# Kernel tuning notes

Hardware: AMD Instinct MI355X
Metric: run time of the kernel (lower is better)

Reference implementation:

```python
import jax, jax.numpy as jnp
import numpy as np

NA = 3            # anchors per scale
NC = 80           # num classes
THRESH = 0.6      # wh-IoU anchor-match threshold
EPS = 1e-7

ANCHORS_PX = np.array([[12,16],[19,36],[40,28],[36,75],[76,55],[72,146],
                       [142,110],[192,243],[459,401]], dtype=np.float32).reshape(3, 3, 2)


def setup_inputs() -> dict:
    key = jax.random.key(0)
    k1, k2, k3, k4, k5, k6 = jax.random.split(key, 6)
    B, M = 16, 32
    p0 = jax.random.normal(k1, (B, NA * (5 + NC), 80, 80), jnp.float32)
    p1 = jax.random.normal(k2, (B, NA * (5 + NC), 40, 40), jnp.float32)
    p2 = jax.random.normal(k3, (B, NA * (5 + NC), 20, 20), jnp.float32)
    # targets: [B, M, 6] = (img_idx, class in [1,NC], cx, cy, w, h) normalized to [0,1]
    bidx = jnp.broadcast_to(jnp.arange(B, dtype=jnp.float32)[:, None], (B, M))
    cls = jax.random.randint(k4, (B, M), 1, NC + 1).astype(jnp.float32)
    xy = jax.random.uniform(k5, (B, M, 2), minval=0.05, maxval=0.95)
    ka, kj = jax.random.split(k6)
    aidx = jax.random.randint(ka, (B, M), 0, 9)
    base_wh = jnp.asarray(ANCHORS_PX.reshape(9, 2))[aidx] / 640.0
    jitter = jnp.exp(jax.random.uniform(kj, (B, M, 2), minval=-0.15, maxval=0.15))
    wh = base_wh * jitter
    targets = jnp.concatenate([bidx[..., None], cls[..., None], xy, wh], axis=-1)
    return {"p0": p0, "p1": p1, "p2": p2,
            "targets": targets,
            "anchors": jnp.asarray(ANCHORS_PX),
            "image_size": jnp.array([640.0, 640.0], jnp.float32)}


def _bce_logits(x, t):
    # BCEWithLogits, pos_weight=1, elementwise
    return jnp.maximum(x, 0.0) - x * t + jnp.log1p(jnp.exp(-jnp.abs(x)))


def _giou(pbox, tbox):
    # boxes [N,4] in cxcywh
    px1 = pbox[:, 0] - pbox[:, 2] * 0.5
    py1 = pbox[:, 1] - pbox[:, 3] * 0.5
    px2 = pbox[:, 0] + pbox[:, 2] * 0.5
    py2 = pbox[:, 1] + pbox[:, 3] * 0.5
    tx1 = tbox[:, 0] - tbox[:, 2] * 0.5
    ty1 = tbox[:, 1] - tbox[:, 3] * 0.5
    tx2 = tbox[:, 0] + tbox[:, 2] * 0.5
    ty2 = tbox[:, 1] + tbox[:, 3] * 0.5
    iw = jnp.clip(jnp.minimum(px2, tx2) - jnp.maximum(px1, tx1), 0.0)
    ih = jnp.clip(jnp.minimum(py2, ty2) - jnp.maximum(py1, ty1), 0.0)
    inter = iw * ih
    union = pbox[:, 2] * pbox[:, 3] + tbox[:, 2] * tbox[:, 3] - inter + EPS
    iou = inter / union
    cw = jnp.maximum(px2, tx2) - jnp.minimum(px1, tx1)
    ch = jnp.maximum(py2, ty2) - jnp.minimum(py1, ty1)
    c_area = cw * ch + EPS
    return iou - (c_area - union) / c_area


def _scale_losses(pi, tflat, anchors_i, image_size):
    # pi: [B, NA*(5+NC), H, W]; tflat: [N,6]; anchors_i: [NA,2] in pixels
    B = pi.shape[0]
    H, W = pi.shape[-2:]
    stride = image_size / jnp.array([H, W], jnp.float32)          # (sH, sW)
    anchor = anchors_i / stride[::-1][None, :]                    # anchors in grid units (w,h)
    gain = jnp.concatenate([jnp.ones((2,), jnp.float32),
                            (1.0 / stride)[jnp.array([1, 0, 1, 0])]])
    t = tflat * gain                                              # [N,6]
    gwh = t[:, 4:6]
    # wh-IoU matrix [NA, N] -> best anchor per target
    inter = (jnp.minimum(anchor[:, None, 0], gwh[None, :, 0])
             * jnp.minimum(anchor[:, None, 1], gwh[None, :, 1]))
    union = anchor[:, None, 0] * anchor[:, None, 1] + gwh[None, :, 0] * gwh[None, :, 1] - inter
    iou = inter / union
    best = iou.max(0)
    a = iou.argmax(0)
    mask = best > THRESH                                          # fixed-shape mask replaces torch boolean compaction
    maskf = mask.astype(jnp.float32)

    b = jnp.where(mask, t[:, 0].astype(jnp.int32), 0)
    c = t[:, 1].astype(jnp.int32)
    gxy = t[:, 2:4]
    gi = jnp.where(mask, gxy[:, 0].astype(jnp.int32), 0)
    gj = jnp.where(mask, gxy[:, 1].astype(jnp.int32), 0)
    a_s = jnp.where(mask, a, 0)

    pir = pi.reshape(B, NA, 5 + NC, H, W).transpose(0, 1, 3, 4, 2)  # [B,NA,H,W,5+NC]
    ps = pir[b, a_s, gj, gi]                                        # [N,5+NC]
    tobj = jnp.zeros((B, NA, H, W), jnp.float32)
    tobj = tobj.at[b, a_s, gj, gi].max(jax.lax.stop_gradient(maskf))

    pxy = jax.nn.sigmoid(ps[:, 0:2])
    pwh = jnp.minimum(jnp.exp(ps[:, 2:4]), 1000.0) * anchor[a_s]
    pbox = jnp.concatenate([pxy, pwh], 1)
    tbox = jnp.concatenate([gxy % 1.0, t[:, 4:6]], 1)
    giou = _giou(pbox, tbox)
    nb = jnp.maximum(maskf.sum(), 1.0)
    lbox = (maskf * (1.0 - giou)).sum() / nb
    tcls = jax.nn.one_hot(c - 1, NC, dtype=jnp.float32)             # cp=1, cn=0 (eps=0)
    lcls = (maskf[:, None] * _bce_logits(ps[:, 5:], tcls)).sum() / (nb * NC)
    lobj = _bce_logits(pir[..., 4], tobj).mean()
    return lbox, lobj, lcls


def _total_loss(p0, p1, p2, targets, anchors, image_size):
    tflat = targets.reshape(-1, 6)
    lbox = lobj = lcls = jnp.float32(0.0)
    for i, pi in enumerate([p0, p1, p2]):
        lb, lo, lc = _scale_losses(pi, tflat, anchors[i], image_size)
        lbox = lbox + lb
        lobj = lobj + lo
        lcls = lcls + lc
    lbox = lbox * 3.54
    lobj = lobj * 64.3
    lcls = lcls * 37.4
    return lbox + lobj + lcls, lbox, lobj, lcls


def reference(p0, p1, p2, targets, anchors, image_size):
    return _total_loss(p0, p1, p2, targets, anchors, image_size)
```

## Files before the change

kernel.cpp:

```cpp
#include <hip/hip_runtime.h>
#include <math.h>

#define NAANCH 3
#define NCLS 80
#define BATCH 16
#define NTGT 512
#define CH 85

#define V4_S0 76800
#define V4_S1 19200
#define V4_S2 4800
#define V4_TOT (V4_S0 + V4_S1 + V4_S2)
#define OBJ_BLOCKS 197
#define GRID_BLOCKS (3 + OBJ_BLOCKS)

#define WBOX 3.54f
#define WOBJ 64.3f
#define WCLS 37.4f

__device__ __forceinline__ float bce0(float x) {
    return fmaxf(x, 0.0f) + log1pf(expf(-fabsf(x)));
}

__device__ __forceinline__ float wave_sum(float v) {
    for (int off = 32; off > 0; off >>= 1) v += __shfl_down(v, off, 64);
    return v;
}

__global__ void yolo_loss_kernel(const float* __restrict__ p0,
                                 const float* __restrict__ p1,
                                 const float* __restrict__ p2,
                                 const float* __restrict__ targets,
                                 const float* __restrict__ anchors,
                                 const float* __restrict__ image_size,
                                 float* __restrict__ out) {
    const int tid  = threadIdx.x;
    const int lane = tid & 63;
    const int wid  = tid >> 6;

    __shared__ int   sh_key[NTGT];
    __shared__ int   sh_off[NTGT];
    __shared__ int   sh_ci[NTGT];
    __shared__ unsigned char sh_mk[NTGT];
    __shared__ float red[4][8];

    if (blockIdx.x < 3) {
        const int s = blockIdx.x;
        const int j = tid;
        const int H = (s == 0) ? 80 : ((s == 1) ? 40 : 20);
        const int W = H;
        const int HW = H * W;
        const float* pi = (s == 0) ? p0 : ((s == 1) ? p1 : p2);

        const float stride0 = image_size[0] / (float)H;
        const float stride1 = image_size[1] / (float)W;
        const float gx = 1.0f / stride1;
        const float gy = 1.0f / stride0;

        const float t0 = targets[j * 6 + 0];
        const float t1 = targets[j * 6 + 1];
        const float tx = targets[j * 6 + 2] * gx;
        const float ty = targets[j * 6 + 3] * gy;
        const float gw = targets[j * 6 + 4] * gx;
        const float gh = targets[j * 6 + 5] * gy;

        float best = -1.0f; int abest = 0;
        for (int k = 0; k < NAANCH; ++k) {
            float aw = anchors[(s * NAANCH + k) * 2 + 0] / stride1;
            float ah = anchors[(s * NAANCH + k) * 2 + 1] / stride0;
            float inter = fminf(aw, gw) * fminf(ah, gh);
            float uni = aw * ah + gw * gh - inter;
            float iou = inter / uni;
            if (iou > best) { best = iou; abest = k; }
        }
        const bool  mask  = best > 0.6f;
        const float maskf = mask ? 1.0f : 0.0f;

        int b  = mask ? (int)t0 : 0;
        const int c = (int)t1;
        int gi = mask ? (int)tx : 0;
        int gj = mask ? (int)ty : 0;
        const int a_s = mask ? abest : 0;
        gi = min(max(gi, 0), W - 1);
        gj = min(max(gj, 0), H - 1);
        b  = min(max(b, 0), BATCH - 1);

        const int key = ((b * NAANCH + a_s) * H + gj) * W + gi;
        const int off = (b * (NAANCH * CH) + a_s * CH) * HW + gj * W + gi;

        float lbox_t = 0.0f, ps4 = 0.0f;
        if (mask) {
            const float ps0 = pi[off + 0 * HW];
            const float ps1 = pi[off + 1 * HW];
            const float ps2 = pi[off + 2 * HW];
            const float ps3 = pi[off + 3 * HW];
            ps4 = pi[off + 4 * HW];

            const float aw = anchors[(s * NAANCH + a_s) * 2 + 0] / stride1;
            const float ah = anchors[(s * NAANCH + a_s) * 2 + 1] / stride0;

            const float pxc = 1.0f / (1.0f + expf(-ps0));
            const float pyc = 1.0f / (1.0f + expf(-ps1));
            const float pw  = fminf(expf(ps2), 1000.0f) * aw;
            const float ph  = fminf(expf(ps3), 1000.0f) * ah;
            const float txc = tx - floorf(tx);
            const float tyc = ty - floorf(ty);

            const float px1 = pxc - pw * 0.5f, py1 = pyc - ph * 0.5f;
            const float px2 = pxc + pw * 0.5f, py2 = pyc + ph * 0.5f;
            const float qx1 = txc - gw * 0.5f, qy1 = tyc - gh * 0.5f;
            const float qx2 = txc + gw * 0.5f, qy2 = tyc + gh * 0.5f;
            const float iw = fmaxf(fminf(px2, qx2) - fmaxf(px1, qx1), 0.0f);
            const float ih = fmaxf(fminf(py2, qy2) - fmaxf(py1, qy1), 0.0f);
            const float inter = iw * ih;
            const float uni = pw * ph + gw * gh - inter + 1e-7f;
            const float iou = inter / uni;
            const float cw  = fmaxf(px2, qx2) - fminf(px1, qx1);
            const float chh = fmaxf(py2, qy2) - fminf(py1, qy1);
            const float carea = cw * chh + 1e-7f;
            lbox_t = 1.0f - (iou - (carea - uni) / carea);
        }

        sh_key[j] = key;
        sh_off[j] = off;
        sh_ci[j]  = c - 1;
        sh_mk[j]  = mask ? 1 : 0;
        __syncthreads();

        float corr = 0.0f;
        if (mask) {
            bool dup = false;
            for (int j2 = 0; j2 < j; ++j2)
                if (sh_mk[j2] && sh_key[j2] == key) { dup = true; break; }
            if (!dup) corr = -ps4;
        }

        float v0 = wave_sum(lbox_t);
        float v1 = wave_sum(maskf);
        float v2 = wave_sum(corr);
        if (lane == 0) { red[0][wid] = v0; red[1][wid] = v1; red[2][wid] = v2; }
        __syncthreads();

        float lcls_w = 0.0f;
        for (int j2 = wid; j2 < NTGT; j2 += 8) {
            if (!sh_mk[j2]) continue;
            const int toff = sh_off[j2];
            const int ci   = sh_ci[j2];
            const int k1 = lane;
            float x1 = pi[toff + (5 + k1) * HW];
            float c1 = bce0(x1) - ((k1 == ci) ? x1 : 0.0f);
            float c2 = 0.0f;
            if (lane < NCLS - 64) {
                const int k2 = 64 + lane;
                float x2 = pi[toff + (5 + k2) * HW];
                c2 = bce0(x2) - ((k2 == ci) ? x2 : 0.0f);
            }
            float tsum = wave_sum(c1 + c2);
            if (lane == 0) lcls_w += tsum;
        }
        if (lane == 0) red[3][wid] = lcls_w;
        __syncthreads();

        if (tid == 0) {
            float acc[4] = {0.f, 0.f, 0.f, 0.f};
            for (int w = 0; w < 8; ++w) {
                acc[0] += red[0][w]; acc[1] += red[1][w];
                acc[2] += red[2][w]; acc[3] += red[3][w];
            }
            const float Ns = (s == 0) ? 307200.0f : ((s == 1) ? 76800.0f : 19200.0f);
            const float nb = fmaxf(acc[1], 1.0f);
            const float lbox_c = WBOX * (acc[0] / nb);
            const float lobj_c = WOBJ * (acc[2] / Ns);
            const float lcls_c = WCLS * (acc[3] / (nb * (float)NCLS));
            atomicAdd(&out[1], lbox_c);
            atomicAdd(&out[2], lobj_c);
            atomicAdd(&out[3], lcls_c);
            atomicAdd(&out[0], lbox_c + lobj_c + lcls_c);
        }
    } else {
        const int vb = (blockIdx.x - 3) * 512 + tid;
        float a0 = 0.f, a1 = 0.f, a2 = 0.f;
        if (vb < V4_TOT) {
            const float4* addr; int hw4; int sflag;
            if (vb < V4_S0) {
                const int u = vb;
                const int ba = u / 1600;  hw4 = u - ba * 1600;
                const int b = ba / 3, a = ba - 3 * b;
                addr = (const float4*)(p0 + (size_t)((b * NAANCH + a) * CH + 4) * 6400);
                sflag = 0;
            } else if (vb < V4_S0 + V4_S1) {
                const int u = vb - V4_S0;
                const int ba = u / 400;   hw4 = u - ba * 400;
                const int b = ba / 3, a = ba - 3 * b;
                addr = (const float4*)(p1 + (size_t)((b * NAANCH + a) * CH + 4) * 1600);
                sflag = 1;
            } else {
                const int u = vb - V4_S0 - V4_S1;
                const int ba = u / 100;   hw4 = u - ba * 100;
                const int b = ba / 3, a = ba - 3 * b;
                addr = (const float4*)(p2 + (size_t)((b * NAANCH + a) * CH + 4) * 400);
                sflag = 2;
            }
            float4 x = addr[hw4];
            float v = bce0(x.x) + bce0(x.y) + bce0(x.z) + bce0(x.w);
            if (sflag == 0) a0 = v; else if (sflag == 1) a1 = v; else a2 = v;
        }
        a0 = wave_sum(a0); a1 = wave_sum(a1); a2 = wave_sum(a2);
        if (lane == 0) { red[0][wid] = a0; red[1][wid] = a1; red[2][wid] = a2; }
        __syncthreads();
        if (tid == 0) {
            float s0 = 0.f, s1 = 0.f, s2 = 0.f;
            for (int w = 0; w < 8; ++w) { s0 += red[0][w]; s1 += red[1][w]; s2 += red[2][w]; }
            const float lobj_c = WOBJ * (s0 / 307200.0f + s1 / 76800.0f + s2 / 19200.0f);
            atomicAdd(&out[2], lobj_c);
            atomicAdd(&out[0], lobj_c);
        }
    }
}

extern "C" void kernel_launch(void* const* d_in, const int* in_sizes, int n_in,
                              void* d_out, int out_size, void* d_ws, size_t ws_size,
                              hipStream_t stream) {
    const float* p0       = (const float*)d_in[0];
    const float* p1       = (const float*)d_in[1];
    const float* p2       = (const float*)d_in[2];
    const float* targets  = (const float*)d_in[3];
    const float* anchors  = (const float*)d_in[4];
    const float* img_size = (const float*)d_in[5];
    float* out = (float*)d_out;

    yolo_loss_kernel<<<GRID_BLOCKS, 512, 0, stream>>>(p0, p1, p2, targets, anchors, img_size, out);
}
```

Measured before the change: 153.4 us.

## Split class-loss gathers across 96 blocks and double objectness work per thread

Moves the per-target class BCE loss out of the three per-scale blocks into 96 dedicated blocks (32 per scale). Each block recomputes the anchor assignment and handles 16 targets with two independent gathers per wave, so the long serial gather loop no longer sits on the critical path. The objectness blocks now process two float4 vectors per thread, halving their count. Assignment math is recomputed redundantly in every class block, and there are more atomics on the output.

```diff
diff --git a/kernel.cpp b/kernel.cpp
--- a/kernel.cpp
+++ b/kernel.cpp
@@ -11,8 +11,12 @@
 #define V4_S1 19200
 #define V4_S2 4800
 #define V4_TOT (V4_S0 + V4_S1 + V4_S2)
-#define OBJ_BLOCKS 197
-#define GRID_BLOCKS (3 + OBJ_BLOCKS)
+
+#define NCB 32
+#define CLS_BASE 3
+#define OBJ_BASE (CLS_BASE + 3 * NCB)
+#define OBJ_BLOCKS 99
+#define GRID_BLOCKS (OBJ_BASE + OBJ_BLOCKS)
 
 #define WBOX 3.54f
 #define WOBJ 64.3f
@@ -27,13 +31,51 @@
     return v;
 }
 
-__global__ void yolo_loss_kernel(const float* __restrict__ p0,
-                                 const float* __restrict__ p1,
-                                 const float* __restrict__ p2,
-                                 const float* __restrict__ targets,
-                                 const float* __restrict__ anchors,
-                                 const float* __restrict__ image_size,
-                                 float* __restrict__ out) {
+__device__ __forceinline__ void compute_assign(
+    const int s, const int j,
+    const float* __restrict__ targets, const float* __restrict__ anchors,
+    const float inv_sx, const float inv_sy,
+    const int H, const int W, const int HW,
+    bool& mask, int& key, int& off, int& ci, int& a_s,
+    float& tx, float& ty, float& gw, float& gh)
+{
+    const float t0 = targets[j * 6 + 0];
+    const float t1 = targets[j * 6 + 1];
+    tx = targets[j * 6 + 2] * inv_sx;
+    ty = targets[j * 6 + 3] * inv_sy;
+    gw = targets[j * 6 + 4] * inv_sx;
+    gh = targets[j * 6 + 5] * inv_sy;
+
+    float best = -1.0f; int abest = 0;
+    for (int k = 0; k < NAANCH; ++k) {
+        const float aw = anchors[(s * NAANCH + k) * 2 + 0] * inv_sx;
+        const float ah = anchors[(s * NAANCH + k) * 2 + 1] * inv_sy;
+        const float inter = fminf(aw, gw) * fminf(ah, gh);
+        const float uni = aw * ah + gw * gh - inter;
+        const float iou = inter / uni;
+        if (iou > best) { best = iou; abest = k; }
+    }
+    mask = best > 0.6f;
+    int b  = mask ? (int)t0 : 0;
+    ci = (int)t1 - 1;
+    int gi = mask ? (int)tx : 0;
+    int gj = mask ? (int)ty : 0;
+    a_s = mask ? abest : 0;
+    gi = min(max(gi, 0), W - 1);
+    gj = min(max(gj, 0), H - 1);
+    b  = min(max(b, 0), BATCH - 1);
+    key = ((b * NAANCH + a_s) * H + gj) * W + gi;
+    off = (b * (NAANCH * CH) + a_s * CH) * HW + gj * W + gi;
+}
+
+__global__ __launch_bounds__(512)
+void yolo_loss_kernel(const float* __restrict__ p0,
+                      const float* __restrict__ p1,
+                      const float* __restrict__ p2,
+                      const float* __restrict__ targets,
+                      const float* __restrict__ anchors,
+                      const float* __restrict__ image_size,
+                      float* __restrict__ out) {
     const int tid  = threadIdx.x;
     const int lane = tid & 63;
     const int wid  = tid >> 6;
@@ -44,49 +86,20 @@
     __shared__ unsigned char sh_mk[NTGT];
     __shared__ float red[4][8];
 
-    if (blockIdx.x < 3) {
+    if (blockIdx.x < CLS_BASE) {
         const int s = blockIdx.x;
         const int j = tid;
         const int H = (s == 0) ? 80 : ((s == 1) ? 40 : 20);
         const int W = H;
         const int HW = H * W;
         const float* pi = (s == 0) ? p0 : ((s == 1) ? p1 : p2);
-
-        const float stride0 = image_size[0] / (float)H;
-        const float stride1 = image_size[1] / (float)W;
-        const float gx = 1.0f / stride1;
-        const float gy = 1.0f / stride0;
-
-        const float t0 = targets[j * 6 + 0];
-        const float t1 = targets[j * 6 + 1];
-        const float tx = targets[j * 6 + 2] * gx;
-        const float ty = targets[j * 6 + 3] * gy;
-        const float gw = targets[j * 6 + 4] * gx;
-        const float gh = targets[j * 6 + 5] * gy;
-
-        float best = -1.0f; int abest = 0;
-        for (int k = 0; k < NAANCH; ++k) {
-            float aw = anchors[(s * NAANCH + k) * 2 + 0] / stride1;
-            float ah = anchors[(s * NAANCH + k) * 2 + 1] / stride0;
-            float inter = fminf(aw, gw) * fminf(ah, gh);
-            float uni = aw * ah + gw * gh - inter;
-            float iou = inter / uni;
-            if (iou > best) { best = iou; abest = k; }
-        }
-        const bool  mask  = best > 0.6f;
+        const float inv_sx = (float)W / image_size[1];
+        const float inv_sy = (float)H / image_size[0];
+
+        bool mask; int key, off, ci, a_s; float tx, ty, gw, gh;
+        compute_assign(s, j, targets, anchors, inv_sx, inv_sy, H, W, HW,
+                       mask, key, off, ci, a_s, tx, ty, gw, gh);
         const float maskf = mask ? 1.0f : 0.0f;
-
-        int b  = mask ? (int)t0 : 0;
-        const int c = (int)t1;
-        int gi = mask ? (int)tx : 0;
-        int gj = mask ? (int)ty : 0;
-        const int a_s = mask ? abest : 0;
-        gi = min(max(gi, 0), W - 1);
-        gj = min(max(gj, 0), H - 1);
-        b  = min(max(b, 0), BATCH - 1);
-
-        const int key = ((b * NAANCH + a_s) * H + gj) * W + gi;
-        const int off = (b * (NAANCH * CH) + a_s * CH) * HW + gj * W + gi;
 
         float lbox_t = 0.0f, ps4 = 0.0f;
         if (mask) {
@@ -96,8 +109,8 @@
             const float ps3 = pi[off + 3 * HW];
             ps4 = pi[off + 4 * HW];
 
-            const float aw = anchors[(s * NAANCH + a_s) * 2 + 0] / stride1;
-            const float ah = anchors[(s * NAANCH + a_s) * 2 + 1] / stride0;
+            const float aw = anchors[(s * NAANCH + a_s) * 2 + 0] * inv_sx;
+            const float ah = anchors[(s * NAANCH + a_s) * 2 + 1] * inv_sy;
 
             const float pxc = 1.0f / (1.0f + expf(-ps0));
             const float pyc = 1.0f / (1.0f + expf(-ps1));
@@ -122,8 +135,6 @@
         }
 
         sh_key[j] = key;
-        sh_off[j] = off;
-        sh_ci[j]  = c - 1;
         sh_mk[j]  = mask ? 1 : 0;
         __syncthreads();
 
@@ -141,69 +152,110 @@
         if (lane == 0) { red[0][wid] = v0; red[1][wid] = v1; red[2][wid] = v2; }
         __syncthreads();
 
-        float lcls_w = 0.0f;
-        for (int j2 = wid; j2 < NTGT; j2 += 8) {
-            if (!sh_mk[j2]) continue;
-            const int toff = sh_off[j2];
-            const int ci   = sh_ci[j2];
-            const int k1 = lane;
-            float x1 = pi[toff + (5 + k1) * HW];
-            float c1 = bce0(x1) - ((k1 == ci) ? x1 : 0.0f);
-            float c2 = 0.0f;
-            if (lane < NCLS - 64) {
-                const int k2 = 64 + lane;
-                float x2 = pi[toff + (5 + k2) * HW];
-                c2 = bce0(x2) - ((k2 == ci) ? x2 : 0.0f);
+        if (tid == 0) {
+            float acc0 = 0.f, acc1 = 0.f, acc2 = 0.f;
+            for (int w = 0; w < 8; ++w) {
+                acc0 += red[0][w]; acc1 += red[1][w]; acc2 += red[2][w];
             }
-            float tsum = wave_sum(c1 + c2);
-            if (lane == 0) lcls_w += tsum;
-        }
-        if (lane == 0) red[3][wid] = lcls_w;
-        __syncthreads();
-
-        if (tid == 0) {
-            float acc[4] = {0.f, 0.f, 0.f, 0.f};
-            for (int w = 0; w < 8; ++w) {
-                acc[0] += red[0][w]; acc[1] += red[1][w];
-                acc[2] += red[2][w]; acc[3] += red[3][w];
-            }
-            const float Ns = (s == 0) ? 307200.0f : ((s == 1) ? 76800.0f : 19200.0f);
-            const float nb = fmaxf(acc[1], 1.0f);
-            const float lbox_c = WBOX * (acc[0] / nb);
-            const float lobj_c = WOBJ * (acc[2] / Ns);
-            const float lcls_c = WCLS * (acc[3] / (nb * (float)NCLS));
+            const float Ns = (float)(48 * HW);
+            const float nb = fmaxf(acc1, 1.0f);
+            const float lbox_c = WBOX * (acc0 / nb);
+            const float lobj_c = WOBJ * (acc2 / Ns);
             atomicAdd(&out[1], lbox_c);
             atomicAdd(&out[2], lobj_c);
+            atomicAdd(&out[0], lbox_c + lobj_c);
+        }
+    } else if (blockIdx.x < OBJ_BASE) {
+        const int cb = blockIdx.x - CLS_BASE;
+        const int s  = cb >> 5;
+        const int g  = cb & 31;
+        const int H = (s == 0) ? 80 : ((s == 1) ? 40 : 20);
+        const int W = H;
+        const int HW = H * W;
+        const float* pi = (s == 0) ? p0 : ((s == 1) ? p1 : p2);
+        const float inv_sx = (float)W / image_size[1];
+        const float inv_sy = (float)H / image_size[0];
+
+        bool mask; int key, off, ci, a_s; float tx, ty, gw, gh;
+        compute_assign(s, tid, targets, anchors, inv_sx, inv_sy, H, W, HW,
+                       mask, key, off, ci, a_s, tx, ty, gw, gh);
+        sh_off[tid] = off;
+        sh_ci[tid]  = ci;
+        sh_mk[tid]  = mask ? 1 : 0;
+        float v1 = wave_sum(mask ? 1.0f : 0.0f);
+        if (lane == 0) red[1][wid] = v1;
+        __syncthreads();
+
+        const int jA = g * 16 + wid;
+        const int jB = jA + 8;
+        const bool mA = sh_mk[jA] != 0;
+        const bool mB = sh_mk[jB] != 0;
+        const int offA = sh_off[jA], ciA = sh_ci[jA];
+        const int offB = sh_off[jB], ciB = sh_ci[jB];
+
+        float x1A = 0.f, x2A = 0.f, x1B = 0.f, x2B = 0.f;
+        if (mA) {
+            x1A = pi[offA + (5 + lane) * HW];
+            if (lane < NCLS - 64) x2A = pi[offA + (69 + lane) * HW];
+        }
+        if (mB) {
+            x1B = pi[offB + (5 + lane) * HW];
+            if (lane < NCLS - 64) x2B = pi[offB + (69 + lane) * HW];
+        }
+        float cA = 0.f, cB = 0.f;
+        if (mA) {
+            cA = bce0(x1A) - ((lane == ciA) ? x1A : 0.0f);
+            if (lane < NCLS - 64)
+                cA += bce0(x2A) - ((lane + 64 == ciA) ? x2A : 0.0f);
+        }
+        if (mB) {
+            cB = bce0(x1B) - ((lane == ciB) ? x1B : 0.0f);
+            if (lane < NCLS - 64)
+                cB += bce0(x2B) - ((lane + 64 == ciB) ? x2B : 0.0f);
+        }
+        const float tsum = wave_sum(cA + cB);
+        if (lane == 0) red[3][wid] = tsum;
+        __syncthreads();
+
+        if (tid == 0) {
+            float nb = 0.f, lc = 0.f;
+            for (int w = 0; w < 8; ++w) { nb += red[1][w]; lc += red[3][w]; }
+            nb = fmaxf(nb, 1.0f);
+            const float lcls_c = WCLS * (lc / (nb * (float)NCLS));
             atomicAdd(&out[3], lcls_c);
-            atomicAdd(&out[0], lbox_c + lobj_c + lcls_c);
+            atomicAdd(&out[0], lcls_c);
         }
     } else {
-        const int vb = (blockIdx.x - 3) * 512 + tid;
+        const int base = (blockIdx.x - OBJ_BASE) * 1024 + tid;
         float a0 = 0.f, a1 = 0.f, a2 = 0.f;
-        if (vb < V4_TOT) {
-            const float4* addr; int hw4; int sflag;
-            if (vb < V4_S0) {
-                const int u = vb;
-                const int ba = u / 1600;  hw4 = u - ba * 1600;
-                const int b = ba / 3, a = ba - 3 * b;
-                addr = (const float4*)(p0 + (size_t)((b * NAANCH + a) * CH + 4) * 6400);
-                sflag = 0;
-            } else if (vb < V4_S0 + V4_S1) {
-                const int u = vb - V4_S0;
-                const int ba = u / 400;   hw4 = u - ba * 400;
-                const int b = ba / 3, a = ba - 3 * b;
-                addr = (const float4*)(p1 + (size_t)((b * NAANCH + a) * CH + 4) * 1600);
-                sflag = 1;
-            } else {
-                const int u = vb - V4_S0 - V4_S1;
-                const int ba = u / 100;   hw4 = u - ba * 100;
-                const int b = ba / 3, a = ba - 3 * b;
-                addr = (const float4*)(p2 + (size_t)((b * NAANCH + a) * CH + 4) * 400);
-                sflag = 2;
+        #pragma unroll
+        for (int t = 0; t < 2; ++t) {
+            const int vb = base + t * 512;
+            if (vb < V4_TOT) {
+                const float4* addr; int hw4; int sflag;
+                if (vb < V4_S0) {
+                    const int u = vb;
+                    const int ba = u / 1600;  hw4 = u - ba * 1600;
+                    const int b = ba / 3, a = ba - 3 * b;
+                    addr = (const float4*)(p0 + (size_t)((b * NAANCH + a) * CH + 4) * 6400);
+                    sflag = 0;
+                } else if (vb < V4_S0 + V4_S1) {
+                    const int u = vb - V4_S0;
+                    const int ba = u / 400;   hw4 = u - ba * 400;
+                    const int b = ba / 3, a = ba - 3 * b;
+                    addr = (const float4*)(p1 + (size_t)((b * NAANCH + a) * CH + 4) * 1600);
+                    sflag = 1;
+                } else {
+                    const int u = vb - V4_S0 - V4_S1;
+                    const int ba = u / 100;   hw4 = u - ba * 100;
+                    const int b = ba / 3, a = ba - 3 * b;
+                    addr = (const float4*)(p2 + (size_t)((b * NAANCH + a) * CH + 4) * 400);
+                    sflag = 2;
+                }
+                float4 x = addr[hw4];
+                float v = bce0(x.x) + bce0(x.y) + bce0(x.z) + bce0(x.w);
+                if (sflag == 0) a0 += v; else if (sflag == 1) a1 += v; else a2 += v;
             }
-            float4 x = addr[hw4];
-            float v = bce0(x.x) + bce0(x.y) + bce0(x.z) + bce0(x.w);
-            if (sflag == 0) a0 = v; else if (sflag == 1) a1 = v; else a2 = v;
         }
         a0 = wave_sum(a0); a1 = wave_sum(a1); a2 = wave_sum(a2);
         if (lane == 0) { red[0][wid] = a0; red[1][wid] = a1; red[2][wid] = a2; }
```

Measured after the change: 153.3 us. Within noise of the previous version (-0.0%).
